# Optimization experiments

Hardware: AMD Instinct MI355X
Metric: run time of the kernel (lower is better)

Reference implementation:

```python
import jax, jax.numpy as jnp
import numpy as np

NEG_SLOPE = 0.01  # nn.LeakyReLU default used in module

def leaky_relu(x):
    return jnp.where(x >= 0, x, NEG_SLOPE * x)

def setup_inputs() -> dict:
    key = jax.random.key(0)
    k1, k2, k3, k4, k5 = jax.random.split(key, 5)
    B, S, D, H, E = 4, 2048, 1024, 2048, 8
    s_in = 1.0 / np.sqrt(D)
    return {
        "inputs": jax.random.normal(k1, (B, S, D), dtype=jnp.float32),
        "Wg": jax.random.normal(k2, (E, D), dtype=jnp.float32) * s_in,
        "bg": jax.random.normal(k3, (E,), dtype=jnp.float32) * s_in,
        "We": jax.random.normal(k4, (E, H, D), dtype=jnp.float32) * s_in,
        "be": jax.random.normal(k5, (E, H), dtype=jnp.float32) * s_in,
    }

def reference(inputs, Wg, bg, We, be):
    # gate: [B,S,E]
    gate_logits = jnp.einsum('bsd,ed->bse', inputs, Wg) + bg
    gate_probs = jax.nn.softmax(gate_logits, axis=-1)
    # all experts densely: [B,S,E,H]
    expert_out = leaky_relu(jnp.einsum('bsd,ehd->bseh', inputs, We) + be)
    # gate-weighted reduction over experts: [B,S,H]
    weighted = jnp.einsum('bseh,bse->bsh', expert_out, gate_probs)
    return weighted
```

## Files before the change

### kernel.cpp

```cpp
#include <hip/hip_runtime.h>
#include <hip/hip_bf16.h>
#include <math.h>

#define M_TOK 8192
#define N_H   2048
#define K_D   1024
#define N_E   8

typedef __bf16 bf16x8 __attribute__((ext_vector_type(8)));
typedef __bf16 bf16x4 __attribute__((ext_vector_type(4)));
typedef float  f32x4  __attribute__((ext_vector_type(4)));

__device__ inline f32x4 mfma16(bf16x8 a, bf16x8 b, f32x4 c) {
  return __builtin_amdgcn_mfma_f32_16x16x32_bf16(a, b, c, 0, 0, 0);
}

__device__ inline void load16_lds(const void* g, void* l) {
  __builtin_amdgcn_global_load_lds(
      (const __attribute__((address_space(1))) void*)g,
      (__attribute__((address_space(3))) void*)l, 16, 0, 0);
}

__global__ __launch_bounds__(256) void cvt_kernel(const float* __restrict__ src,
                                                  __bf16* __restrict__ dst,
                                                  int n4) {
  int i = blockIdx.x * blockDim.x + threadIdx.x;
  const int stride = gridDim.x * blockDim.x;
  for (; i < n4; i += stride) {
    float4 v = ((const float4*)src)[i];
    bf16x4 o = {(__bf16)v.x, (__bf16)v.y, (__bf16)v.z, (__bf16)v.w};
    *(bf16x4*)(dst + (size_t)i * 4) = o;
  }
}

__global__ __launch_bounds__(256) void gate_kernel(const float* __restrict__ X,
                                                   const float* __restrict__ Wg,
                                                   const float* __restrict__ bg,
                                                   float* __restrict__ gate,
                                                   __bf16* __restrict__ Xb) {
  const int tid = threadIdx.x;
  const int lane = tid & 63;
  const int wv = tid >> 6;
  const int token = blockIdx.x * 4 + wv;
  const float* xrow = X + (size_t)token * K_D;

  float xr[16];
#pragma unroll
  for (int i = 0; i < 16; ++i) xr[i] = xrow[lane + i * 64];

#pragma unroll
  for (int i = 0; i < 16; ++i)
    Xb[(size_t)token * K_D + lane + i * 64] = (__bf16)xr[i];

  float l[N_E];
#pragma unroll
  for (int e = 0; e < N_E; ++e) {
    const float* wrow = Wg + e * K_D;
    float s = 0.f;
#pragma unroll
    for (int i = 0; i < 16; ++i) s += xr[i] * wrow[lane + i * 64];
#pragma unroll
    for (int off = 32; off > 0; off >>= 1) s += __shfl_xor(s, off);
    l[e] = s + bg[e];
  }
  float mx = l[0];
#pragma unroll
  for (int e = 1; e < N_E; ++e) mx = fmaxf(mx, l[e]);
  float p[N_E], den = 0.f;
#pragma unroll
  for (int e = 0; e < N_E; ++e) { p[e] = expf(l[e] - mx); den += p[e]; }
  const float inv = 1.f / den;
  if (lane == 0) {
#pragma unroll
    for (int e = 0; e < N_E; ++e) gate[(size_t)token * N_E + e] = p[e] * inv;
  }
}

__global__ __launch_bounds__(512, 2) void moe_main(
    const __bf16* __restrict__ Xb, const __bf16* __restrict__ Wb,
    const float* __restrict__ gate, const float* __restrict__ be,
    float* __restrict__ out) {
  __shared__ __bf16 As[4][8192];
  __shared__ __bf16 Bs[4][8192];
  __shared__ float gS[256 * 8];
  __shared__ float bS[8 * 128];

  const int tid = threadIdx.x;
  const int lane = tid & 63;
  const int wv = tid >> 6;
  const int wm = wv >> 1;
  const int wn = wv & 1;
  const int row0 = blockIdx.x * 256;
  const int col0 = blockIdx.y * 128;

  for (int i = tid; i < 2048; i += 512) gS[i] = gate[(size_t)row0 * N_E + i];
  for (int i = tid; i < 1024; i += 512)
    bS[i] = be[(size_t)(i >> 7) * N_H + col0 + (i & 127)];

  const int rA = tid >> 2;
  const int kk = (tid & 3) * 8;
  const __bf16* aB = Xb + (size_t)(row0 + rA) * K_D + kk;
  const __bf16* bB = Wb + (size_t)(col0 + rA) * K_D + kk;

  const int lr = lane & 15;
  const int lk = (lane >> 4) * 8;
  const int aOff = (wm * 64 + lr) * 32 + lk;
  const int bOff = (wn * 64 + lr) * 32 + lk;

  f32x4 fin[4][4];
#pragma unroll
  for (int m = 0; m < 4; ++m)
#pragma unroll
    for (int h = 0; h < 4; ++h) fin[m][h] = (f32x4){0.f, 0.f, 0.f, 0.f};

  f32x4 acc[4][8];
#pragma unroll
  for (int m = 0; m < 4; ++m)
#pragma unroll
    for (int n = 0; n < 8; ++n) acc[m][n] = (f32x4){0.f, 0.f, 0.f, 0.f};

  auto STAGE = [&](int sn, int q) {
    const int k0 = (sn & 31) << 5;
    const size_t pOff = (size_t)(sn >> 5) << 22;
    load16_lds(aB + k0, &As[q][tid * 8]);
    load16_lds(aB + (size_t)128 * K_D + k0, &As[q][4096 + tid * 8]);
    load16_lds(bB + pOff + k0, &Bs[q][tid * 8]);
    load16_lds(bB + pOff + (size_t)N_H * K_D + k0, &Bs[q][4096 + tid * 8]);
  };

  auto EPI = [&](int p) {
    const int e0 = p * 2;
#pragma unroll
    for (int m = 0; m < 4; ++m) {
#pragma unroll
      for (int j = 0; j < 4; ++j) {
        const int r = wm * 64 + m * 16 + (lane >> 4) * 4 + j;
        const float g0 = gS[r * 8 + e0];
        const float g1 = gS[r * 8 + e0 + 1];
#pragma unroll
        for (int h = 0; h < 4; ++h) {
          const int c = wn * 64 + h * 16 + lr;
          float v0 = acc[m][h][j] + bS[e0 * 128 + c];
          v0 = (v0 >= 0.f) ? v0 : 0.01f * v0;
          float v1 = acc[m][4 + h][j] + bS[(e0 + 1) * 128 + c];
          v1 = (v1 >= 0.f) ? v1 : 0.01f * v1;
          fin[m][h][j] += g0 * v0 + g1 * v1;
        }
      }
    }
#pragma unroll
    for (int m = 0; m < 4; ++m)
#pragma unroll
      for (int n = 0; n < 8; ++n) acc[m][n] = (f32x4){0.f, 0.f, 0.f, 0.f};
  };

  auto PHASE = [&](int sn, int q, bool doStage, bool lastPhase) {
    if (lastPhase)
      asm volatile("s_waitcnt vmcnt(0)" ::: "memory");
    else
      asm volatile("s_waitcnt vmcnt(4)" ::: "memory");
    __builtin_amdgcn_s_barrier();
    __builtin_amdgcn_sched_barrier(0);

    bf16x8 af[4], bfr[8];
#pragma unroll
    for (int m = 0; m < 4; ++m)
      af[m] = *(const bf16x8*)(&As[q][aOff + m * 512]);
#pragma unroll
    for (int n = 0; n < 8; ++n)
      bfr[n] = *(const bf16x8*)(&Bs[q][bOff + ((n >> 2) * 128 + (n & 3) * 16) * 32]);
    asm volatile("s_waitcnt lgkmcnt(0)" ::: "memory");
    __builtin_amdgcn_sched_barrier(0);

    if (doStage) STAGE(sn + 2, (q + 2) & 3);

    __builtin_amdgcn_s_setprio(1);
#pragma unroll
    for (int n = 0; n < 8; ++n)
#pragma unroll
      for (int m = 0; m < 4; ++m)
        acc[m][n] = mfma16(af[m], bfr[n], acc[m][n]);
    __builtin_amdgcn_s_setprio(0);

    if ((sn & 31) == 31) EPI(sn >> 5);
  };

  STAGE(0, 0);
  STAGE(1, 1);

#pragma unroll 1
  for (int t4 = 0; t4 < 31; ++t4) {
    const int sn = t4 * 4;
    PHASE(sn + 0, 0, true, false);
    PHASE(sn + 1, 1, true, false);
    PHASE(sn + 2, 2, true, false);
    PHASE(sn + 3, 3, true, false);
  }
  PHASE(124, 0, true, false);
  PHASE(125, 1, true, false);
  PHASE(126, 2, false, false);
  PHASE(127, 3, false, true);

#pragma unroll
  for (int m = 0; m < 4; ++m) {
#pragma unroll
    for (int j = 0; j < 4; ++j) {
      const size_t r = (size_t)(row0 + wm * 64 + m * 16 + (lane >> 4) * 4 + j);
#pragma unroll
      for (int h = 0; h < 4; ++h) {
        out[r * N_H + col0 + wn * 64 + h * 16 + lr] = fin[m][h][j];
      }
    }
  }
}

extern "C" void kernel_launch(void* const* d_in, const int* in_sizes, int n_in,
                              void* d_out, int out_size, void* d_ws, size_t ws_size,
                              hipStream_t stream) {
  const float* X  = (const float*)d_in[0];
  const float* Wg = (const float*)d_in[1];
  const float* bg = (const float*)d_in[2];
  const float* We = (const float*)d_in[3];
  const float* be = (const float*)d_in[4];
  float* out = (float*)d_out;

  char* ws = (char*)d_ws;
  __bf16* Xb   = (__bf16*)(ws);
  __bf16* Wb   = (__bf16*)(ws + (size_t)16 * 1024 * 1024);
  float*  gate = (float*)(ws + (size_t)48 * 1024 * 1024);

  cvt_kernel<<<2048, 256, 0, stream>>>(We, Wb, (N_E * N_H * K_D) / 4);

  gate_kernel<<<M_TOK / 4, 256, 0, stream>>>(X, Wg, bg, gate, Xb);

  dim3 grid(M_TOK / 256, N_H / 128);
  moe_main<<<grid, 512, 0, stream>>>(Xb, Wb, gate, be, out);
}
```

Baseline: 304.5 us.

## Double-buffer MFMA operand fragments in registers to overlap LDS reads with MFMA

The main loop is restructured so that each step loads the LDS fragments for the current k-stage into one register set while the MFMAs run on the previous stage's fragments held in a second set. The prologue and epilogue are shifted to match, and the expert epilogue now fires one step later. The goal is to hide LDS read latency behind the MFMA chain instead of waiting on lgkmcnt before each batch. In exchange it keeps two fragment sets live (24 bf16x8 registers), which raises register pressure and may cause spills or lower occupancy.

```diff
diff --git a/kernel.cpp b/kernel.cpp
--- a/kernel.cpp
+++ b/kernel.cpp
@@ -119,6 +119,8 @@
 #pragma unroll
     for (int n = 0; n < 8; ++n) acc[m][n] = (f32x4){0.f, 0.f, 0.f, 0.f};
 
+  bf16x8 fE[12], fO[12];
+
   auto STAGE = [&](int sn, int q) {
     const int k0 = (sn & 31) << 5;
     const size_t pOff = (size_t)(sn >> 5) << 22;
@@ -154,52 +156,60 @@
       for (int n = 0; n < 8; ++n) acc[m][n] = (f32x4){0.f, 0.f, 0.f, 0.f};
   };
 
-  auto PHASE = [&](int sn, int q, bool doStage, bool lastPhase) {
-    if (lastPhase)
-      asm volatile("s_waitcnt vmcnt(0)" ::: "memory");
-    else
-      asm volatile("s_waitcnt vmcnt(4)" ::: "memory");
-    __builtin_amdgcn_s_barrier();
-    __builtin_amdgcn_sched_barrier(0);
-
-    bf16x8 af[4], bfr[8];
-#pragma unroll
-    for (int m = 0; m < 4; ++m)
-      af[m] = *(const bf16x8*)(&As[q][aOff + m * 512]);
-#pragma unroll
-    for (int n = 0; n < 8; ++n)
-      bfr[n] = *(const bf16x8*)(&Bs[q][bOff + ((n >> 2) * 128 + (n & 3) * 16) * 32]);
-    asm volatile("s_waitcnt lgkmcnt(0)" ::: "memory");
-    __builtin_amdgcn_sched_barrier(0);
-
-    if (doStage) STAGE(sn + 2, (q + 2) & 3);
-
-    __builtin_amdgcn_s_setprio(1);
-#pragma unroll
-    for (int n = 0; n < 8; ++n)
-#pragma unroll
-      for (int m = 0; m < 4; ++m)
-        acc[m][n] = mfma16(af[m], bfr[n], acc[m][n]);
-    __builtin_amdgcn_s_setprio(0);
-
-    if ((sn & 31) == 31) EPI(sn >> 5);
-  };
+#define RDF(q, F)                                                           \
+  do {                                                                      \
+    _Pragma("unroll") for (int m = 0; m < 4; ++m)                           \
+        F[m] = *(const bf16x8*)(&As[q][aOff + m * 512]);                    \
+    _Pragma("unroll") for (int n = 0; n < 8; ++n)                           \
+        F[4 + n] =                                                          \
+            *(const bf16x8*)(&Bs[q][bOff + ((n >> 2) * 128 + (n & 3) * 16) * 32]); \
+  } while (0)
+
+#define MFM(F)                                                              \
+  do {                                                                      \
+    __builtin_amdgcn_s_setprio(1);                                          \
+    _Pragma("unroll") for (int n = 0; n < 8; ++n)                           \
+        _Pragma("unroll") for (int m = 0; m < 4; ++m)                       \
+            acc[m][n] = mfma16(F[m], F[4 + n], acc[m][n]);                  \
+    __builtin_amdgcn_s_setprio(0);                                          \
+  } while (0)
+
+#define STEPP(sn, q, RF, MF_, doStage, last)                                \
+  do {                                                                      \
+    if (last)                                                               \
+      asm volatile("s_waitcnt vmcnt(0)" ::: "memory");                      \
+    else                                                                    \
+      asm volatile("s_waitcnt vmcnt(4)" ::: "memory");                      \
+    __builtin_amdgcn_s_barrier();                                           \
+    __builtin_amdgcn_sched_barrier(0);                                      \
+    RDF(q, RF);                                                             \
+    if (doStage) STAGE((sn) + 2, ((q) + 2) & 3);                            \
+    __builtin_amdgcn_sched_barrier(0);                                      \
+    MFM(MF_);                                                               \
+    if (((sn) & 31) == 0 && (sn) > 0) EPI(((sn) - 1) >> 5);                 \
+  } while (0)
 
   STAGE(0, 0);
   STAGE(1, 1);
+  asm volatile("s_waitcnt vmcnt(4)" ::: "memory");
+  __builtin_amdgcn_s_barrier();
+  __builtin_amdgcn_sched_barrier(0);
+  RDF(0, fE);
+  STAGE(2, 2);
 
 #pragma unroll 1
-  for (int t4 = 0; t4 < 31; ++t4) {
-    const int sn = t4 * 4;
-    PHASE(sn + 0, 0, true, false);
-    PHASE(sn + 1, 1, true, false);
-    PHASE(sn + 2, 2, true, false);
-    PHASE(sn + 3, 3, true, false);
-  }
-  PHASE(124, 0, true, false);
-  PHASE(125, 1, true, false);
-  PHASE(126, 2, false, false);
-  PHASE(127, 3, false, true);
+  for (int t = 0; t < 31; ++t) {
+    const int sn = 1 + t * 4;
+    STEPP(sn + 0, 1, fO, fE, true, false);
+    STEPP(sn + 1, 2, fE, fO, true, false);
+    STEPP(sn + 2, 3, fO, fE, true, false);
+    STEPP(sn + 3, 0, fE, fO, true, false);
+  }
+  STEPP(125, 1, fO, fE, true,  false);
+  STEPP(126, 2, fE, fO, false, false);
+  STEPP(127, 3, fO, fE, false, true);
+  MFM(fO);
+  EPI(3);
 
 #pragma unroll
   for (int m = 0; m < 4; ++m) {
@@ -212,6 +222,9 @@
       }
     }
   }
+#undef RDF
+#undef MFM
+#undef STEPP
 }
 
 extern "C" void kernel_launch(void* const* d_in, const int* in_sizes, int n_in,
```

New measurement: 683.4 us. 2.24x slower.
